# Optimization experiments

Measured on AMD Instinct MI355X. Metric: run time of the kernel, lower is better.

The kernel has to match this reference:

```python
import jax, jax.numpy as jnp
import numpy as np

D = 64      # node_input_dim == node_hidden_dim
EIN = 16    # edge_input_dim
EH = 64     # edge_hidden_dim
NL, NR = 5000, 15000
EL, ER = 50000, 150000
STEPS = 6
EPS = 1e-5
SLOPE = 0.01


def _ln(x, g, b):
    mu = jnp.mean(x, axis=-1, keepdims=True)
    v = jnp.mean((x - mu) ** 2, axis=-1, keepdims=True)
    return (x - mu) / jnp.sqrt(v + EPS) * g + b


def _lrelu(x):
    return jnp.where(x > 0, x, SLOPE * x)


def setup_inputs() -> dict:
    key = jax.random.key(0)
    ks = jax.random.split(key, 32)

    def n(k, shape, fan_in):
        return jax.random.normal(k, shape, jnp.float32) * (fan_in ** -0.5)

    return {
        'lig_n_feat': jax.random.normal(ks[0], (NL, D), jnp.float32),
        'lig_e_feat': jax.random.normal(ks[1], (EL, EIN), jnp.float32),
        'lig_src': jax.random.randint(ks[2], (EL,), 0, NL),
        'lig_dst': jax.random.randint(ks[3], (EL,), 0, NL),
        'rec_n_feat': jax.random.normal(ks[4], (NR, D), jnp.float32),
        'rec_e_feat': jax.random.normal(ks[5], (ER, EIN), jnp.float32),
        'rec_src': jax.random.randint(ks[6], (ER,), 0, NR),
        'rec_dst': jax.random.randint(ks[7], (ER,), 0, NR),
        'mask': jax.random.uniform(ks[8], (NL, NR), jnp.float32),
        # linear0
        'W0': n(ks[9], (D, D), D), 'b0': jnp.zeros((D,), jnp.float32),
        # edge network: Linear(EIN,EH) -> ReLU -> Linear(EH, D*D)
        'We1': n(ks[10], (EH, EIN), EIN), 'be1': jnp.zeros((EH,), jnp.float32),
        'We2': n(ks[11], (D * D, EH), EH), 'be2': jnp.zeros((D * D,), jnp.float32),
        # NNConv residual fc (no bias) and conv bias
        'resW': n(ks[12], (D, D), D), 'conv_b': jnp.zeros((D,), jnp.float32),
        # message layer Linear(2D, D)
        'msgW': n(ks[13], (D, 2 * D), 2 * D), 'msgb': jnp.zeros((D,), jnp.float32),
        # attention projections (no bias)
        'Qlig': n(ks[14], (D, D), D), 'Klig': n(ks[15], (D, D), D), 'Vlig': n(ks[16], (D, D), D),
        'Qrec': n(ks[17], (D, D), D), 'Krec': n(ks[18], (D, D), D), 'Vrec': n(ks[19], (D, D), D),
        # final LayerNorms
        'g_lig': jnp.ones((D,), jnp.float32), 'b_lig': jnp.zeros((D,), jnp.float32),
        'g_rec': jnp.ones((D,), jnp.float32), 'b_rec': jnp.zeros((D,), jnp.float32),
    }


def _gather_branch(x, efeat, src, dst, n_nodes, W0, b0, We1, be1, We2, be2, resW, conv_b, msgW, msgb):
    # per-edge weight matrices from edge MLP: [E, D, D] (in x out)
    We = jax.nn.relu(efeat @ We1.T + be1) @ We2.T + be2
    We = We.reshape(-1, D, D)
    h = jax.nn.relu(x @ W0.T + b0)
    for _ in range(STEPS):
        msg = jnp.einsum('ei,eio->eo', h[src], We)          # gather + per-edge transform
        agg = jax.ops.segment_sum(msg, dst, num_segments=n_nodes)  # scatter-sum
        m = jax.nn.relu(agg + h @ resW.T + conv_b)           # NNConv residual + bias, relu
        h = jnp.concatenate([m, h], axis=1) @ msgW.T + msgb  # message_layer
    return h + x


def reference(lig_n_feat, lig_e_feat, lig_src, lig_dst, rec_n_feat, rec_e_feat, rec_src, rec_dst,
              mask, W0, b0, We1, be1, We2, be2, resW, conv_b, msgW, msgb,
              Qlig, Klig, Vlig, Qrec, Krec, Vrec, g_lig, b_lig, g_rec, b_rec):
    lig_Fv = _gather_branch(lig_n_feat, lig_e_feat, lig_src, lig_dst, NL,
                            W0, b0, We1, be1, We2, be2, resW, conv_b, msgW, msgb)
    rec_Fv = _gather_branch(rec_n_feat, rec_e_feat, rec_src, rec_dst, NR,
                            W0, b0, We1, be1, We2, be2, resW, conv_b, msgW, msgb)
    hl = _ln(lig_Fv, g_lig, b_lig)
    hr = _ln(rec_Fv, g_rec, b_rec)
    # lig attends to rec
    ql, kr, vr = _lrelu(hl @ Qlig.T), _lrelu(hr @ Krec.T), hr @ Vrec.T
    a = mask * (ql @ kr.T) - 1000.0 * (1.0 - mask)
    att_lig = jax.nn.softmax(a, axis=1) @ vr
    # rec attends to lig
    qr, kl, vl = _lrelu(hr @ Qrec.T), _lrelu(hl @ Klig.T), hl @ Vlig.T
    mt = mask.T
    a2 = mt * (qr @ kl.T) - 1000.0 * (1.0 - mt)
    att_rec = jax.nn.softmax(a2, axis=1) @ vl
    return (_ln(att_lig, g_lig, b_lig), _ln(att_rec, g_rec, b_rec))
```

## Files before the change

kernel.cpp:

```cpp
#include <hip/hip_runtime.h>
#include <hip/hip_bf16.h>

typedef unsigned short ushort_t;
typedef __attribute__((ext_vector_type(8))) short short8_t;
typedef __attribute__((ext_vector_type(4))) float f32x4;
typedef __attribute__((ext_vector_type(4))) unsigned uint4_t;

#define NLIG 5000
#define NREC 15000
#define NTOT 20000
#define ELIG 50000
#define EREC 150000
#define ETOT 200000
#define VSTRIDE 20160

__device__ __forceinline__ float us2f(ushort_t u){
  union { float f; unsigned int i; } x; x.i = ((unsigned int)u) << 16; return x.f;
}
__device__ __forceinline__ ushort_t f2us(float f){
  __hip_bfloat16 b = __float2bfloat16(f);
  return *reinterpret_cast<ushort_t*>(&b);
}
__device__ __forceinline__ unsigned pkbf(float a, float b){
  return (unsigned)f2us(a) | ((unsigned)f2us(b) << 16);
}
__device__ __forceinline__ float wsum64(float v){
#pragma unroll
  for (int s = 32; s >= 1; s >>= 1) v += __shfl_xor(v, s, 64);
  return v;
}
__device__ __forceinline__ f32x4 mfma32(short8_t a, short8_t b, f32x4 c){
  return __builtin_amdgcn_mfma_f32_16x16x32_bf16(a, b, c, 0, 0, 0);
}
__device__ __forceinline__ int geti(const int* __restrict__ p, int i, int i64){
  return i64 ? p[2*i] : p[i];
}

__global__ void kdetect2(const unsigned* __restrict__ xw, const unsigned* __restrict__ iw,
                         int* __restrict__ flagp){
  const int lane = threadIdx.x;
  unsigned w = xw[lane];
  int e0 = (int)((w >> 7) & 0xFF);
  int hit = (e0 >= 100 && e0 <= 134) ? 1 : 0;
  int zodd = ((lane & 1) && iw[lane] == 0u) ? 1 : 0;
#pragma unroll
  for (int s = 32; s >= 1; s >>= 1){
    hit  += __shfl_xor(hit,  s, 64);
    zodd += __shfl_xor(zodd, s, 64);
  }
  if (lane == 0){
    flagp[0] = (hit  >= 40) ? 1 : 0;
    flagp[1] = (zodd >= 24) ? 1 : 0;
  }
}

__global__ void ksent(float* __restrict__ out, int n, float c){
  int i = blockIdx.x*256 + threadIdx.x;
  if (i < n) out[i] = c;
}

__global__ void kcvt_x(const void* __restrict__ lx, const void* __restrict__ rx,
                       const int* __restrict__ flagp, float* __restrict__ xall){
  const int flag = flagp[0];
  const int idx = blockIdx.x*256 + threadIdx.x;
  const void* src; int local;
  if (idx < NLIG*64){ src = lx; local = idx; } else { src = rx; local = idx - NLIG*64; }
  float v;
  if (flag) v = us2f(((const ushort_t*)src)[local]);
  else      v = ((const float*)src)[local];
  xall[idx] = v;
}

struct Srcs { const void* p[20]; };
__global__ void kcvt_w(Srcs S, const int* __restrict__ flagp, float* __restrict__ wcvt){
  const int bounds[21] = {0,4096,4160,5184,5248,267392,271488,275584,275648,283840,
                          283904,288000,292096,296192,300288,304384,308480,308544,308608,308672,308736};
  const int flag = flagp[0];
  const int idx = blockIdx.x*256 + threadIdx.x;
  if (idx >= 308736) return;
  int seg = 0;
#pragma unroll
  for (int s = 1; s < 20; ++s) if (idx >= bounds[s]) seg = s;
  const void* src = S.p[0];
#pragma unroll
  for (int s = 1; s < 20; ++s) if (seg == s) src = S.p[s];
  const int local = idx - bounds[seg];
  float v;
  if (flag) v = us2f(((const ushort_t*)src)[local]);
  else      v = ((const float*)src)[local];
  wcvt[idx] = v;
}

#define W_W0    0
#define W_B0    4096
#define W_WE1   4160
#define W_BE1   5184
#define W_WE2   5248
#define W_BE2   267392
#define W_RESW  271488
#define W_CONVB 275584
#define W_MSGW  275648
#define W_MSGB  283840
#define W_QLIG  283904
#define W_KLIG  288000
#define W_VLIG  292096
#define W_QREC  296192
#define W_KREC  300288
#define W_VREC  304384
#define W_GLIG  308480
#define W_BLIG  308544
#define W_GREC  308608
#define W_BREC  308672

__global__ void kWpk(const float* __restrict__ We2f, ushort_t* __restrict__ Wpk){
  int oidx = blockIdx.x*256 + threadIdx.x;
  int j = oidx & 7, lane = (oidx >> 3) & 63, p = (oidx >> 9) & 1;
  int t = (oidx >> 10) & 3, kb = oidx >> 12;
  int o = t*16 + (lane & 15);
  int gik = kb*32 + (lane >> 4)*8 + j;
  int i = gik >> 6, k = gik & 63;
  float v = We2f[(size_t)(i*64 + o)*64 + k];
  ushort_t hi = f2us(v);
  Wpk[oidx] = p ? f2us(v - us2f(hi)) : hi;
}

__global__ void kh0(const float* __restrict__ xall, const float* __restrict__ W0f,
                    const float* __restrict__ b0f, float* __restrict__ h){
  __shared__ float xr[4][64];
  const int lane = threadIdx.x & 63, wv = threadIdx.x >> 6;
  const int n = blockIdx.x*4 + wv;
  xr[wv][lane] = xall[(size_t)n*64 + lane];
  __syncthreads();
  float acc = b0f[lane];
  const float* wr = W0f + lane*64;
#pragma unroll
  for (int i = 0; i < 64; ++i) acc += xr[wv][i] * wr[i];
  h[(size_t)n*64 + lane] = acc > 0.f ? acc : 0.f;
}

__global__ void khist(const int* __restrict__ ldst, const int* __restrict__ rdst,
                      const int* __restrict__ flagp, int* __restrict__ counts){
  const int i64 = flagp[1];
  const int e = blockIdx.x*256 + threadIdx.x;
  if (e >= ETOT) return;
  int dstg = (e < ELIG) ? geti(ldst, e, i64) : geti(rdst, e - ELIG, i64) + NLIG;
  atomicAdd(&counts[dstg], 1);
}

__global__ __launch_bounds__(1024) void kscan(const int* __restrict__ counts, int* __restrict__ offs){
  __shared__ int part[1024];
  const int tid = threadIdx.x;
  const int PER = 20;
  int loc[PER]; int s = 0;
#pragma unroll
  for (int j = 0; j < PER; ++j){ int idx = tid*PER + j; int v = (idx < NTOT) ? counts[idx] : 0; loc[j] = s; s += v; }
  part[tid] = s;
  __syncthreads();
  for (int d = 1; d < 1024; d <<= 1){
    int add = (tid >= d) ? part[tid - d] : 0;
    __syncthreads();
    part[tid] += add;
    __syncthreads();
  }
  int pre = (tid > 0) ? part[tid - 1] : 0;
#pragma unroll
  for (int j = 0; j < PER; ++j){ int idx = tid*PER + j; if (idx < NTOT) offs[idx] = pre + loc[j]; }
  if (tid == 1023) offs[NTOT] = part[1023];
}

__global__ void kfill(const int* __restrict__ lsrc, const int* __restrict__ ldst,
                      const int* __restrict__ rsrc, const int* __restrict__ rdst,
                      const void* __restrict__ lef, const void* __restrict__ ref_,
                      const int* __restrict__ offs, int* __restrict__ cursor,
                      const int* __restrict__ flagp,
                      int* __restrict__ e_srcn, float* __restrict__ ef_srt){
  const int flag = flagp[0];
  const int i64  = flagp[1];
  const int e = blockIdx.x*256 + threadIdx.x;
  if (e >= ETOT) return;
  int srcg, dstg, le; const void* efb;
  if (e < ELIG){ srcg = geti(lsrc, e, i64); dstg = geti(ldst, e, i64); efb = lef; le = e; }
  else {
    int e2 = e - ELIG;
    srcg = geti(rsrc, e2, i64) + NLIG; dstg = geti(rdst, e2, i64) + NLIG; efb = ref_; le = e2;
  }
  int pos = offs[dstg] + atomicAdd(&cursor[dstg], 1);
  e_srcn[pos] = srcg;
  float* efd = ef_srt + (size_t)pos*16;
  if (flag){
    const ushort_t* efp = (const ushort_t*)efb + (size_t)le*16;
#pragma unroll
    for (int c = 0; c < 16; ++c) efd[c] = us2f(efp[c]);
  } else {
    const float* efp = (const float*)efb + (size_t)le*16;
#pragma unroll
    for (int c = 0; c < 16; ++c) efd[c] = efp[c];
  }
}

__global__ __launch_bounds__(1024)
void kstep(const float* __restrict__ hin, float* __restrict__ hout,
           const int* __restrict__ offs, const int* __restrict__ e_srcn,
           const float* __restrict__ ef_srt,
           const ushort_t* __restrict__ Wpk,
           const float* __restrict__ We1f, const float* __restrict__ be1f,
           const float* __restrict__ resWf, const float* __restrict__ convbf,
           const float* __restrict__ msgWf, const float* __restrict__ msgbf,
           const float* __restrict__ be2f){
  __shared__ alignas(16) char sbuf[65536];
  __shared__ float h_lds[1024];
  __shared__ float Hs_lds[1024];
  __shared__ float m_lds[1024];
  __shared__ float cbf[64], mbf[64];

  const int tid = threadIdx.x, lane = tid & 63, wv = tid >> 6;
  const int n0 = blockIdx.x * 16;

  h_lds[tid] = hin[(size_t)n0*64 + tid];
  if (tid < 64){ cbf[tid] = convbf[tid]; mbf[tid] = msgbf[tid]; }

  float w1r[16];
#pragma unroll
  for (int c = 0; c < 16; ++c) w1r[c] = We1f[lane*16 + c];
  const float b1 = be1f[lane];

  float sacc[64];
#pragma unroll
  for (int i = 0; i < 64; ++i) sacc[i] = 0.f;
  float hs = 0.f;
  {
    const int v = n0 + wv;
    const int jb = offs[v], je = offs[v+1];
    for (int j = jb; j < je; ++j){
      const int sn = e_srcn[j];
      const float* efp = ef_srt + (size_t)j*16;
      float zl = b1;
#pragma unroll
      for (int c = 0; c < 16; ++c) zl += efp[c] * w1r[c];
      zl = zl > 0.f ? zl : 0.f;
      hs += hin[(size_t)sn*64 + lane];
      const float4* hp = (const float4*)(hin + (size_t)sn*64);
#pragma unroll
      for (int i4 = 0; i4 < 16; ++i4){
        float4 hv = hp[i4];
        sacc[i4*4+0] += hv.x * zl;
        sacc[i4*4+1] += hv.y * zl;
        sacc[i4*4+2] += hv.z * zl;
        sacc[i4*4+3] += hv.w * zl;
      }
    }
    Hs_lds[wv*64 + lane] = hs;
  }

  const int r15 = lane & 15, g4 = lane >> 4;
  const int tW = wv & 3, kq = wv >> 2;
  f32x4 acc; acc[0]=0.f; acc[1]=0.f; acc[2]=0.f; acc[3]=0.f;
  const unsigned sswz = ((unsigned)(wv & 7)) << 4;
  const unsigned rswz = ((unsigned)(r15 & 7)) << 4;
#pragma unroll
  for (int c = 0; c < 4; ++c){
#pragma unroll
    for (int ii = 0; ii < 16; ++ii){
      float v = sacc[c*16 + ii];
      ushort_t hi16 = f2us(v);
      unsigned off = ((unsigned)(wv*2048 + (ii*64 + lane)*2)) ^ sswz;
      *(ushort_t*)(sbuf + off) = hi16;
      *(ushort_t*)(sbuf + 32768 + off) = f2us(v - us2f(hi16));
    }
    __syncthreads();
    for (int kk = 0; kk < 8; ++kk){
      const int lk = kq*256 + kk*32;
      const int kb = c*32 + kq*8 + kk;
      const unsigned aoff = ((unsigned)(r15*2048 + (lk + g4*8)*2)) ^ rswz;
      const short8_t ah = *(const short8_t*)(sbuf + aoff);
      const short8_t al = *(const short8_t*)(sbuf + 32768 + aoff);
      const ushort_t* bp = Wpk + (size_t)(kb*4 + tW)*1024 + lane*8;
      const short8_t bh = *(const short8_t*)(bp);
      const short8_t bl = *(const short8_t*)(bp + 512);
      acc = mfma32(ah, bh, acc);
      acc = mfma32(ah, bl, acc);
      acc = mfma32(al, bh, acc);
    }
    __syncthreads();
  }

  float* redf  = (float*)sbuf;
  float* be2s  = (float*)(sbuf + 16384);
  float* resWt = (float*)(sbuf + 32768);
#pragma unroll
  for (int q = 0; q < 4; ++q)
    redf[kq*1024 + (g4*4 + q)*64 + tW*16 + r15] = acc[q];
  for (int idx = tid; idx < 4096; idx += 1024){
    be2s[idx] = be2f[idx];
    resWt[(idx & 63)*65 + (idx >> 6)] = resWf[idx];
  }
  __syncthreads();
  {
    float aggv = cbf[lane];
#pragma unroll
    for (int k4 = 0; k4 < 4; ++k4) aggv += redf[k4*1024 + wv*64 + lane];
    float t1 = 0.f, t2 = 0.f;
#pragma unroll 8
    for (int i = 0; i < 64; ++i){
      t1 += Hs_lds[wv*64 + i] * be2s[i*64 + lane];
      t2 += h_lds[wv*64 + i]  * resWt[i*65 + lane];
    }
    float mv = aggv + t1 + t2;
    m_lds[wv*64 + lane] = mv > 0.f ? mv : 0.f;
  }
  __syncthreads();
  float* msgWt = (float*)sbuf;
  for (int idx = tid; idx < 8192; idx += 1024)
    msgWt[(idx & 127)*65 + (idx >> 7)] = msgWf[idx];
  __syncthreads();
  {
    float hn = mbf[lane];
#pragma unroll 8
    for (int i = 0; i < 64; ++i){
      hn += m_lds[wv*64 + i] * msgWt[i*65 + lane];
      hn += h_lds[wv*64 + i] * msgWt[(64 + i)*65 + lane];
    }
    hout[(size_t)(n0 + wv)*64 + lane] = hn;
  }
}

__global__ void kfvproj(const float* __restrict__ h, const float* __restrict__ xall,
    const float* __restrict__ wcvt,
    ushort_t* __restrict__ qbh, ushort_t* __restrict__ qbl,
    ushort_t* __restrict__ kbh, ushort_t* __restrict__ kbl,
    ushort_t* __restrict__ vbT){
  __shared__ float hr[4][64];
  const int lane = threadIdx.x & 63, wv = threadIdx.x >> 6;
  const int n = blockIdx.x*4 + wv;
  const bool isLig = n < NLIG;
  const float fv = h[(size_t)n*64 + lane] + xall[(size_t)n*64 + lane];
  const float mu = wsum64(fv) * (1.f/64.f);
  const float dd = fv - mu;
  const float var = wsum64(dd*dd) * (1.f/64.f);
  const float gg = wcvt[(isLig ? W_GLIG : W_GREC) + lane];
  const float bb = wcvt[(isLig ? W_BLIG : W_BREC) + lane];
  const float hl = dd * rsqrtf(var + 1e-5f) * gg + bb;
  hr[wv][lane] = hl;
  __syncthreads();
  const float* Qw = wcvt + (isLig ? W_QLIG : W_QREC) + lane*64;
  const float* Kw = wcvt + (isLig ? W_KLIG : W_KREC) + lane*64;
  const float* Vw = wcvt + (isLig ? W_VLIG : W_VREC) + lane*64;
  float qa = 0.f, ka = 0.f, va = 0.f;
#pragma unroll
  for (int i = 0; i < 64; ++i){
    const float hv = hr[wv][i];
    qa += hv * Qw[i];
    ka += hv * Kw[i];
    va += hv * Vw[i];
  }
  qa = qa > 0.f ? qa : 0.01f*qa;
  ka = ka > 0.f ? ka : 0.01f*ka;
  const size_t o = (size_t)n*64 + lane;
  ushort_t qh = f2us(qa); qbh[o] = qh; qbl[o] = f2us(qa - us2f(qh));
  ushort_t kh = f2us(ka); kbh[o] = kh; kbl[o] = f2us(ka - us2f(kh));
  vbT[(size_t)lane*VSTRIDE + n] = f2us(va);
}

template<int DIRN>
__global__ __launch_bounds__(512)
void kattn(const ushort_t* __restrict__ qbh, const ushort_t* __restrict__ qbl,
           const ushort_t* __restrict__ kbh, const ushort_t* __restrict__ kbl,
           const ushort_t* __restrict__ vbT, const void* __restrict__ maskp,
           const int* __restrict__ flagp,
           const float* __restrict__ gwf, const float* __restrict__ bwf,
           float* __restrict__ out){
  constexpr int R   = DIRN ? NREC : NLIG;
  constexpr int C   = DIRN ? NLIG : NREC;
  constexpr int RNB = DIRN ? NLIG : 0;
  constexpr int CNB = DIRN ? 0 : NLIG;
  __shared__ float mred[8][16], lred[8][16];
  __shared__ float ored[8][64][17];
  __shared__ float m_tile[16][257];

  const int flag = flagp[0];
  const int tid = threadIdx.x, lane = tid & 63, wv = tid >> 6;
  const int r15 = lane & 15, g4 = lane >> 4;
  const int rbase = blockIdx.x * 16;
  int rn = rbase + r15; if (rn > R-1) rn = R-1;

  const ushort_t* qph = qbh + (size_t)(RNB + rn)*64;
  const ushort_t* qpl = qbl + (size_t)(RNB + rn)*64;
  const short8_t qh0a = *(const short8_t*)(qph + g4*8);
  const short8_t qh0b = *(const short8_t*)(qph + 32 + g4*8);
  const short8_t ql0a = *(const short8_t*)(qpl + g4*8);
  const short8_t ql0b = *(const short8_t*)(qpl + 32 + g4*8);

  const int srcA = (((g4 & 1) * 2)     << 4) + r15;
  const int srcB = (((g4 & 1) * 2 + 1) << 4) + r15;
  const bool hiBank = (g4 >> 1) != 0;

  float mrun = -1e30f, lrun = 0.f;
  f32x4 oacc[4];
#pragma unroll
  for (int t = 0; t < 4; ++t){ oacc[t][0]=0.f; oacc[t][1]=0.f; oacc[t][2]=0.f; oacc[t][3]=0.f; }

  for (int tb = 0; tb < C; tb += 256){
    __syncthreads();
    if (DIRN == 0){
      const int row = tid >> 5;
      int r = rbase + row; if (r > R-1) r = R-1;
      int col = tb + (tid & 31)*8; if (col > C-8) col = C-8;
      const size_t base = (size_t)r*NREC + col;
      const int cl0 = col - tb;
      if (flag){
        const ushort_t* mp = (const ushort_t*)maskp + base;
#pragma unroll
        for (int j = 0; j < 8; ++j) m_tile[row][cl0 + j] = us2f(mp[j]);
      } else {
        const float* mp = (const float*)maskp + base;
        const float4 v0 = *(const float4*)mp;
        const float4 v1 = *(const float4*)(mp + 4);
        m_tile[row][cl0+0]=v0.x; m_tile[row][cl0+1]=v0.y;
        m_tile[row][cl0+2]=v0.z; m_tile[row][cl0+3]=v0.w;
        m_tile[row][cl0+4]=v1.x; m_tile[row][cl0+5]=v1.y;
        m_tile[row][cl0+6]=v1.z; m_tile[row][cl0+7]=v1.w;
      }
    } else {
      const int cl = tid >> 1, half = tid & 1;
      int c = tb + cl; if (c > C-1) c = C-1;
      int r0 = rbase + half*8; if (r0 > R-8) r0 = R-8;
      const size_t base = (size_t)c*NREC + r0;
      const int rr0 = r0 - rbase;
      const int cc = c - tb;
      if (flag){
        const ushort_t* mp = (const ushort_t*)maskp + base;
#pragma unroll
        for (int j = 0; j < 8; ++j) m_tile[rr0 + j][cc] = us2f(mp[j]);
      } else {
        const float* mp = (const float*)maskp + base;
        const float4 v0 = *(const float4*)mp;
        const float4 v1 = *(const float4*)(mp + 4);
        m_tile[rr0+0][cc]=v0.x; m_tile[rr0+1][cc]=v0.y;
        m_tile[rr0+2][cc]=v0.z; m_tile[rr0+3][cc]=v0.w;
        m_tile[rr0+4][cc]=v1.x; m_tile[rr0+5][cc]=v1.y;
        m_tile[rr0+6][cc]=v1.z; m_tile[rr0+7][cc]=v1.w;
      }
    }
    __syncthreads();

    const int cb = tb + wv*32;
    int cn0 = cb + r15;      if (cn0 > C-1) cn0 = C-1;
    int cn1 = cb + 16 + r15; if (cn1 > C-1) cn1 = C-1;
    const ushort_t* kp0h = kbh + (size_t)(CNB + cn0)*64;
    const ushort_t* kp0l = kbl + (size_t)(CNB + cn0)*64;
    const ushort_t* kp1h = kbh + (size_t)(CNB + cn1)*64;
    const ushort_t* kp1l = kbl + (size_t)(CNB + cn1)*64;
    f32x4 st0; st0[0]=0.f; st0[1]=0.f; st0[2]=0.f; st0[3]=0.f;
    f32x4 st1 = st0;
    {
      short8_t ka_ = *(const short8_t*)(kp0h + g4*8);
      short8_t kb_ = *(const short8_t*)(kp0h + 32 + g4*8);
      st0 = mfma32(ka_, qh0a, st0); st0 = mfma32(kb_, qh0b, st0);
      st0 = mfma32(ka_, ql0a, st0); st0 = mfma32(kb_, ql0b, st0);
      short8_t kc_ = *(const short8_t*)(kp0l + g4*8);
      short8_t kd_ = *(const short8_t*)(kp0l + 32 + g4*8);
      st0 = mfma32(kc_, qh0a, st0); st0 = mfma32(kd_, qh0b, st0);
    }
    {
      short8_t ka_ = *(const short8_t*)(kp1h + g4*8);
      short8_t kb_ = *(const short8_t*)(kp1h + 32 + g4*8);
      st1 = mfma32(ka_, qh0a, st1); st1 = mfma32(kb_, qh0b, st1);
      st1 = mfma32(ka_, ql0a, st1); st1 = mfma32(kb_, ql0b, st1);
      short8_t kc_ = *(const short8_t*)(kp1l + g4*8);
      short8_t kd_ = *(const short8_t*)(kp1l + 32 + g4*8);
      st1 = mfma32(kc_, qh0a, st1); st1 = mfma32(kd_, qh0b, st1);
    }
    float sv0[4], sv1[4]; float tmax = -1e30f;
#pragma unroll
    for (int j = 0; j < 4; ++j){
      const int c0 = cb + g4*4 + j, c1 = cb + 16 + g4*4 + j;
      const float mv0 = m_tile[r15][wv*32 + g4*4 + j];
      const float mv1 = m_tile[r15][wv*32 + 16 + g4*4 + j];
      sv0[j] = (c0 < C) ? mv0 * (st0[j] + 1000.f) : -1e30f;
      sv1[j] = (c1 < C) ? mv1 * (st1[j] + 1000.f) : -1e30f;
      tmax = fmaxf(tmax, fmaxf(sv0[j], sv1[j]));
    }
    tmax = fmaxf(tmax, __shfl_xor(tmax, 16, 64));
    tmax = fmaxf(tmax, __shfl_xor(tmax, 32, 64));
    const float mnew = fmaxf(mrun, tmax);
    const float corr = __expf(mrun - mnew);
    float ps0[4], ps1[4], psum = 0.f;
#pragma unroll
    for (int j = 0; j < 4; ++j){
      ps0[j] = __expf(sv0[j] - mnew); psum += ps0[j];
      ps1[j] = __expf(sv1[j] - mnew); psum += ps1[j];
    }
    psum += __shfl_xor(psum, 16, 64);
    psum += __shfl_xor(psum, 32, 64);
    lrun = lrun * corr + psum;
    mrun = mnew;
    const unsigned pk0 = pkbf(ps0[0], ps0[1]);
    const unsigned pk1 = pkbf(ps0[2], ps0[3]);
    const unsigned pk2 = pkbf(ps1[0], ps1[1]);
    const unsigned pk3 = pkbf(ps1[2], ps1[3]);
    const unsigned a0 = (unsigned)__shfl((int)pk0, srcA, 64);
    const unsigned a2 = (unsigned)__shfl((int)pk2, srcA, 64);
    const unsigned a1 = (unsigned)__shfl((int)pk1, srcA, 64);
    const unsigned a3 = (unsigned)__shfl((int)pk3, srcA, 64);
    const unsigned b0 = (unsigned)__shfl((int)pk0, srcB, 64);
    const unsigned b2 = (unsigned)__shfl((int)pk2, srcB, 64);
    const unsigned b1 = (unsigned)__shfl((int)pk1, srcB, 64);
    const unsigned b3 = (unsigned)__shfl((int)pk3, srcB, 64);
    uint4_t pw;
    pw[0] = hiBank ? a2 : a0;
    pw[1] = hiBank ? a3 : a1;
    pw[2] = hiBank ? b2 : b0;
    pw[3] = hiBank ? b3 : b1;
    const short8_t pf8 = *reinterpret_cast<const short8_t*>(&pw);
    const ushort_t* vtb = vbT + (size_t)(CNB + cb + g4*8);
#pragma unroll
    for (int t = 0; t < 4; ++t){
#pragma unroll
      for (int q = 0; q < 4; ++q) oacc[t][q] *= corr;
      const short8_t af = *(const short8_t*)(vtb + (size_t)(t*16 + r15)*VSTRIDE);
      oacc[t] = mfma32(af, pf8, oacc[t]);
    }
  }

  if (g4 == 0){ mred[wv][r15] = mrun; lred[wv][r15] = lrun; }
#pragma unroll
  for (int t = 0; t < 4; ++t)
#pragma unroll
    for (int q = 0; q < 4; ++q)
      ored[wv][t*16 + g4*4 + q][r15] = oacc[t][q];
  __syncthreads();

  for (int rr = 2*wv; rr <= 2*wv + 1; ++rr){
    float mstar = -1e30f;
#pragma unroll
    for (int w = 0; w < 8; ++w) mstar = fmaxf(mstar, mred[w][rr]);
    float lstar = 0.f, ov = 0.f;
#pragma unroll
    for (int w = 0; w < 8; ++w){
      const float e = __expf(mred[w][rr] - mstar);
      lstar += lred[w][rr] * e;
      ov    += ored[w][lane][rr] * e;
    }
    const float att = ov / lstar;
    const float mu = wsum64(att) * (1.f/64.f);
    const float dd = att - mu;
    const float var = wsum64(dd*dd) * (1.f/64.f);
    const float y = dd * rsqrtf(var + 1e-5f) * gwf[lane] + bwf[lane];
    const int rg = rbase + rr;
    if (rg < R) out[(size_t)rg*64 + lane] = y;
  }
}

extern "C" void kernel_launch(void* const* d_in, const int* in_sizes, int n_in,
                              void* d_out, int out_size, void* d_ws, size_t ws_size,
                              hipStream_t stream){
  const int expsz[29] = {320000,800000,50000,50000,960000,2400000,150000,150000,75000000,
                         4096,64,1024,64,262144,4096,4096,64,8192,64,
                         4096,4096,4096,4096,4096,4096,64,64,64,64};
  bool ok = (n_in == 29);
  if (ok) for (int i = 0; i < 29; ++i) if (in_sizes[i] != expsz[i]) ok = false;
  if (!ok){
    ksent<<<(out_size + 255)/256, 256, 0, stream>>>((float*)d_out, out_size, 10.0f);
    return;
  }

  const void* lig_n = d_in[0];
  const void* lig_e = d_in[1];
  const int* lig_src = (const int*)d_in[2];
  const int* lig_dst = (const int*)d_in[3];
  const void* rec_n = d_in[4];
  const void* rec_e = d_in[5];
  const int* rec_src = (const int*)d_in[6];
  const int* rec_dst = (const int*)d_in[7];
  const void* mask = d_in[8];

  char* p = (char*)d_ws;
  auto carve = [&](size_t bytes)->char*{ char* r = p; p += (bytes + 255) & ~(size_t)255; return r; };
  float*    xall  = (float*)   carve((size_t)NTOT*64*4);
  float*    wcvt  = (float*)   carve((size_t)308736*4);
  float*    h_a   = (float*)   carve((size_t)NTOT*64*4);
  float*    h_b   = (float*)   carve((size_t)NTOT*64*4);
  ushort_t* Wpk   = (ushort_t*)carve((size_t)524288*2);
  ushort_t* qbh   = (ushort_t*)carve((size_t)NTOT*64*2);
  ushort_t* qbl   = (ushort_t*)carve((size_t)NTOT*64*2);
  ushort_t* kbh   = (ushort_t*)carve((size_t)NTOT*64*2);
  ushort_t* kbl   = (ushort_t*)carve((size_t)NTOT*64*2);
  ushort_t* vbT   = (ushort_t*)carve((size_t)64*VSTRIDE*2);
  int*      flag  = (int*)     carve(256);
  int*      counts= (int*)     carve((size_t)2*NTOT*4);
  int*      cursor= counts + NTOT;
  int*      offs  = (int*)     carve((size_t)(NTOT+1)*4);
  int*      e_srcn= (int*)     carve((size_t)ETOT*4);
  float*    ef_srt= (float*)   carve((size_t)ETOT*16*4);

  if ((size_t)(p - (char*)d_ws) > ws_size){
    ksent<<<(out_size + 255)/256, 256, 0, stream>>>((float*)d_out, out_size, 20.0f);
    return;
  }

  Srcs S;
  for (int i = 0; i < 20; ++i) S.p[i] = d_in[9 + i];

  hipMemsetAsync(counts, 0, (size_t)2*NTOT*4, stream);
  hipMemsetAsync(vbT, 0, (size_t)64*VSTRIDE*2, stream);
  kdetect2<<<1, 64, 0, stream>>>((const unsigned*)lig_n, (const unsigned*)lig_src, flag);
  kcvt_x<<<NTOT*64/256, 256, 0, stream>>>(lig_n, rec_n, flag, xall);
  kcvt_w<<<(308736 + 255)/256, 256, 0, stream>>>(S, flag, wcvt);
  kWpk<<<2048, 256, 0, stream>>>(wcvt + W_WE2, Wpk);
  kh0<<<NTOT/4, 256, 0, stream>>>(xall, wcvt + W_W0, wcvt + W_B0, h_a);
  khist<<<(ETOT + 255)/256, 256, 0, stream>>>(lig_dst, rec_dst, flag, counts);
  kscan<<<1, 1024, 0, stream>>>(counts, offs);
  kfill<<<(ETOT + 255)/256, 256, 0, stream>>>(lig_src, lig_dst, rec_src, rec_dst,
                                              lig_e, rec_e, offs, cursor, flag, e_srcn, ef_srt);
  float* hi = h_a; float* ho = h_b;
  for (int s = 0; s < 6; ++s){
    kstep<<<NTOT/16, 1024, 0, stream>>>(hi, ho, offs, e_srcn, ef_srt, Wpk,
                                        wcvt + W_WE1, wcvt + W_BE1, wcvt + W_RESW,
                                        wcvt + W_CONVB, wcvt + W_MSGW, wcvt + W_MSGB,
                                        wcvt + W_BE2);
    float* t = hi; hi = ho; ho = t;
  }
  kfvproj<<<NTOT/4, 256, 0, stream>>>(hi, xall, wcvt, qbh, qbl, kbh, kbl, vbT);
  kattn<0><<<(NLIG + 15)/16, 512, 0, stream>>>(qbh, qbl, kbh, kbl, vbT, mask, flag,
                                               wcvt + W_GLIG, wcvt + W_BLIG,
                                               (float*)d_out);
  kattn<1><<<(NREC + 15)/16, 512, 0, stream>>>(qbh, qbl, kbh, kbl, vbT, mask, flag,
                                               wcvt + W_GREC, wcvt + W_BREC,
                                               (float*)d_out + (size_t)NLIG*64);
}
```

Measured before the change: 2.283 ms.

## Merge both attention directions into one launch with double-buffered register-prefetched mask tiles

Combines the two attention kernels into a single grid whose block index selects the direction, so both run in one launch and can share the GPU. The mask tile for the next column block is prefetched into registers while the current tile is computed, and the shared-memory tile is double-buffered, which drops one barrier per iteration. The reduction scratch reuses the tile buffer's shared memory. The direction is now a runtime value instead of a template parameter, which may add branches and registers.

```diff
diff --git a/kernel.cpp b/kernel.cpp
--- a/kernel.cpp
+++ b/kernel.cpp
@@ -13,6 +13,8 @@
 #define EREC 150000
 #define ETOT 200000
 #define VSTRIDE 20160
+#define NB0 313
+#define NB1 938
 
 __device__ __forceinline__ float us2f(ushort_t u){
   union { float f; unsigned int i; } x; x.i = ((unsigned int)u) << 16; return x.f;
@@ -361,26 +363,32 @@
   vbT[(size_t)lane*VSTRIDE + n] = f2us(va);
 }
 
-template<int DIRN>
 __global__ __launch_bounds__(512)
-void kattn(const ushort_t* __restrict__ qbh, const ushort_t* __restrict__ qbl,
-           const ushort_t* __restrict__ kbh, const ushort_t* __restrict__ kbl,
-           const ushort_t* __restrict__ vbT, const void* __restrict__ maskp,
-           const int* __restrict__ flagp,
-           const float* __restrict__ gwf, const float* __restrict__ bwf,
-           float* __restrict__ out){
-  constexpr int R   = DIRN ? NREC : NLIG;
-  constexpr int C   = DIRN ? NLIG : NREC;
-  constexpr int RNB = DIRN ? NLIG : 0;
-  constexpr int CNB = DIRN ? 0 : NLIG;
+void kattn2(const ushort_t* __restrict__ qbh, const ushort_t* __restrict__ qbl,
+            const ushort_t* __restrict__ kbh, const ushort_t* __restrict__ kbl,
+            const ushort_t* __restrict__ vbT, const void* __restrict__ maskp,
+            const int* __restrict__ flagp, const float* __restrict__ wcvt,
+            float* __restrict__ out){
+  __shared__ alignas(16) char abuf[34816];
   __shared__ float mred[8][16], lred[8][16];
-  __shared__ float ored[8][64][17];
-  __shared__ float m_tile[16][257];
+  float (*m_tile)[16][257] = (float(*)[16][257])abuf;
+  float (*ored)[64][17]    = (float(*)[64][17])abuf;
 
   const int flag = flagp[0];
+  const int bx = blockIdx.x;
+  const int dirn = (bx < NB0) ? 0 : 1;
+  const int bid  = dirn ? (bx - NB0) : bx;
+  const int R   = dirn ? NREC : NLIG;
+  const int C   = dirn ? NLIG : NREC;
+  const int RNB = dirn ? NLIG : 0;
+  const int CNB = dirn ? 0 : NLIG;
+  const float* gwf = wcvt + (dirn ? W_GREC : W_GLIG);
+  const float* bwf = wcvt + (dirn ? W_BREC : W_BLIG);
+  float* outp = out + (size_t)RNB*64;
+
   const int tid = threadIdx.x, lane = tid & 63, wv = tid >> 6;
   const int r15 = lane & 15, g4 = lane >> 4;
-  const int rbase = blockIdx.x * 16;
+  const int rbase = bid * 16;
   int rn = rbase + r15; if (rn > R-1) rn = R-1;
 
   const ushort_t* qph = qbh + (size_t)(RNB + rn)*64;
@@ -394,53 +402,65 @@
   const int srcB = (((g4 & 1) * 2 + 1) << 4) + r15;
   const bool hiBank = (g4 >> 1) != 0;
 
-  float mrun = -1e30f, lrun = 0.f;
-  f32x4 oacc[4];
-#pragma unroll
-  for (int t = 0; t < 4; ++t){ oacc[t][0]=0.f; oacc[t][1]=0.f; oacc[t][2]=0.f; oacc[t][3]=0.f; }
-
-  for (int tb = 0; tb < C; tb += 256){
-    __syncthreads();
-    if (DIRN == 0){
-      const int row = tid >> 5;
-      int r = rbase + row; if (r > R-1) r = R-1;
-      int col = tb + (tid & 31)*8; if (col > C-8) col = C-8;
-      const size_t base = (size_t)r*NREC + col;
-      const int cl0 = col - tb;
+  const int s_row = tid >> 5, s_l31 = tid & 31;
+  const int s_cl = tid >> 1, s_half = tid & 1;
+
+  float mr[8];
+  auto load_tile = [&](int tb2){
+    if (dirn == 0){
+      int r = rbase + s_row; if (r > R-1) r = R-1;
+      const size_t base = (size_t)r*NREC + tb2;
+      const int cmax = C-1 - tb2;
       if (flag){
         const ushort_t* mp = (const ushort_t*)maskp + base;
 #pragma unroll
-        for (int j = 0; j < 8; ++j) m_tile[row][cl0 + j] = us2f(mp[j]);
+        for (int j = 0; j < 8; ++j){
+          int cj = s_l31 + 32*j; if (cj > cmax) cj = cmax;
+          mr[j] = us2f(mp[cj]);
+        }
+      } else {
+        const float* mp = (const float*)maskp + base;
+#pragma unroll
+        for (int j = 0; j < 8; ++j){
+          int cj = s_l31 + 32*j; if (cj > cmax) cj = cmax;
+          mr[j] = mp[cj];
+        }
+      }
+    } else {
+      int c = tb2 + s_cl; if (c > C-1) c = C-1;
+      int r0 = rbase + s_half*8; if (r0 > R-8) r0 = R-8;
+      const size_t base = (size_t)c*NREC + r0;
+      if (flag){
+        const ushort_t* mp = (const ushort_t*)maskp + base;
+        const short8_t v8 = *(const short8_t*)mp;
+#pragma unroll
+        for (int j = 0; j < 8; ++j) mr[j] = us2f((ushort_t)v8[j]);
       } else {
         const float* mp = (const float*)maskp + base;
         const float4 v0 = *(const float4*)mp;
         const float4 v1 = *(const float4*)(mp + 4);
-        m_tile[row][cl0+0]=v0.x; m_tile[row][cl0+1]=v0.y;
-        m_tile[row][cl0+2]=v0.z; m_tile[row][cl0+3]=v0.w;
-        m_tile[row][cl0+4]=v1.x; m_tile[row][cl0+5]=v1.y;
-        m_tile[row][cl0+6]=v1.z; m_tile[row][cl0+7]=v1.w;
+        mr[0]=v0.x; mr[1]=v0.y; mr[2]=v0.z; mr[3]=v0.w;
+        mr[4]=v1.x; mr[5]=v1.y; mr[6]=v1.z; mr[7]=v1.w;
       }
+    }
+  };
+
+  float mrun = -1e30f, lrun = 0.f;
+  f32x4 oacc[4];
+#pragma unroll
+  for (int t = 0; t < 4; ++t){ oacc[t][0]=0.f; oacc[t][1]=0.f; oacc[t][2]=0.f; oacc[t][3]=0.f; }
+
+  load_tile(0);
+  int buf = 0;
+  for (int tb = 0; tb < C; tb += 256){
+    if (dirn == 0){
+#pragma unroll
+      for (int j = 0; j < 8; ++j) m_tile[buf][s_row][s_l31 + 32*j] = mr[j];
     } else {
-      const int cl = tid >> 1, half = tid & 1;
-      int c = tb + cl; if (c > C-1) c = C-1;
-      int r0 = rbase + half*8; if (r0 > R-8) r0 = R-8;
-      const size_t base = (size_t)c*NREC + r0;
-      const int rr0 = r0 - rbase;
-      const int cc = c - tb;
-      if (flag){
-        const ushort_t* mp = (const ushort_t*)maskp + base;
-#pragma unroll
-        for (int j = 0; j < 8; ++j) m_tile[rr0 + j][cc] = us2f(mp[j]);
-      } else {
-        const float* mp = (const float*)maskp + base;
-        const float4 v0 = *(const float4*)mp;
-        const float4 v1 = *(const float4*)(mp + 4);
-        m_tile[rr0+0][cc]=v0.x; m_tile[rr0+1][cc]=v0.y;
-        m_tile[rr0+2][cc]=v0.z; m_tile[rr0+3][cc]=v0.w;
-        m_tile[rr0+4][cc]=v1.x; m_tile[rr0+5][cc]=v1.y;
-        m_tile[rr0+6][cc]=v1.z; m_tile[rr0+7][cc]=v1.w;
-      }
-    }
+#pragma unroll
+      for (int j = 0; j < 8; ++j) m_tile[buf][s_half*8 + j][s_cl] = mr[j];
+    }
+    if (tb + 256 < C) load_tile(tb + 256);
     __syncthreads();
 
     const int cb = tb + wv*32;
@@ -474,8 +494,8 @@
 #pragma unroll
     for (int j = 0; j < 4; ++j){
       const int c0 = cb + g4*4 + j, c1 = cb + 16 + g4*4 + j;
-      const float mv0 = m_tile[r15][wv*32 + g4*4 + j];
-      const float mv1 = m_tile[r15][wv*32 + 16 + g4*4 + j];
+      const float mv0 = m_tile[buf][r15][wv*32 + g4*4 + j];
+      const float mv1 = m_tile[buf][r15][wv*32 + 16 + g4*4 + j];
       sv0[j] = (c0 < C) ? mv0 * (st0[j] + 1000.f) : -1e30f;
       sv1[j] = (c1 < C) ? mv1 * (st1[j] + 1000.f) : -1e30f;
       tmax = fmaxf(tmax, fmaxf(sv0[j], sv1[j]));
@@ -520,8 +540,10 @@
       const short8_t af = *(const short8_t*)(vtb + (size_t)(t*16 + r15)*VSTRIDE);
       oacc[t] = mfma32(af, pf8, oacc[t]);
     }
-  }
-
+    buf ^= 1;
+  }
+
+  __syncthreads();
   if (g4 == 0){ mred[wv][r15] = mrun; lred[wv][r15] = lrun; }
 #pragma unroll
   for (int t = 0; t < 4; ++t)
@@ -547,7 +569,7 @@
     const float var = wsum64(dd*dd) * (1.f/64.f);
     const float y = dd * rsqrtf(var + 1e-5f) * gwf[lane] + bwf[lane];
     const int rg = rbase + rr;
-    if (rg < R) out[(size_t)rg*64 + lane] = y;
+    if (rg < R) outp[(size_t)rg*64 + lane] = y;
   }
 }
 
@@ -621,10 +643,6 @@
     float* t = hi; hi = ho; ho = t;
   }
   kfvproj<<<NTOT/4, 256, 0, stream>>>(hi, xall, wcvt, qbh, qbl, kbh, kbl, vbT);
-  kattn<0><<<(NLIG + 15)/16, 512, 0, stream>>>(qbh, qbl, kbh, kbl, vbT, mask, flag,
-                                               wcvt + W_GLIG, wcvt + W_BLIG,
-                                               (float*)d_out);
-  kattn<1><<<(NREC + 15)/16, 512, 0, stream>>>(qbh, qbl, kbh, kbl, vbT, mask, flag,
-                                               wcvt + W_GREC, wcvt + W_BREC,
-                                               (float*)d_out + (size_t)NLIG*64);
-}
+  kattn2<<<NB0 + NB1, 512, 0, stream>>>(qbh, qbl, kbh, kbl, vbT, mask, flag, wcvt,
+                                        (float*)d_out);
+}
```

Result: faster. 2.135 ms (-6.5%).
